# Kernel tuning notes

Hardware: AMD Instinct MI355X
Metric: run time of the kernel (lower is better)

The kernel has to match this reference:

```python
import jax, jax.numpy as jnp
import numpy as np
from jax import lax

B, C, O, K, KS, H, W = 16, 256, 256, 4, 3, 64, 64
PAD = 1
BN_EPS = 1e-3


def setup_inputs() -> dict:
    key = jax.random.key(0)
    k1, k2, k3 = jax.random.split(key, 3)
    x = jax.random.normal(k1, (B, C, H, W), dtype=jnp.float32)
    # nn.Parameter(torch.randn(...)) -> standard normal init
    dyn_kernels = jax.random.normal(k2, (K, O, C, KS, KS), dtype=jnp.float32)
    # attention 1x1 conv (no bias): weight [K, C, 1, 1] -> store as [K, C]
    attn_w = jax.random.normal(k3, (K, C), dtype=jnp.float32) / np.sqrt(C).astype(np.float32)
    gamma = jnp.ones((O,), dtype=jnp.float32)
    beta = jnp.zeros((O,), dtype=jnp.float32)
    return {"x": x, "dyn_kernels": dyn_kernels, "attn_w": attn_w, "gamma": gamma, "beta": beta}


def reference(x, dyn_kernels, attn_w, gamma, beta):
    b, c, h, w = x.shape
    k, o = dyn_kernels.shape[0], dyn_kernels.shape[1]
    # attention: global avg pool -> 1x1 conv (no bias) -> softmax over kernels
    pooled = x.mean(axis=(2, 3))                      # [B, C]
    attn = jax.nn.softmax(pooled @ attn_w.T, axis=1)  # [B, K]
    # run all K kernels as a single conv with K*O output channels
    kern = dyn_kernels.reshape(k * o, c, KS, KS)
    y = lax.conv_general_dilated(
        x, kern, window_strides=(1, 1), padding=((PAD, PAD), (PAD, PAD)),
        dimension_numbers=("NCHW", "OIHW", "NCHW"))   # [B, K*O, H, W]
    y = y.reshape(b, k, o, h, w)
    out = jnp.einsum("bkohw,bk->bohw", y, attn)        # weighted sum over kernels
    # BatchNorm2d (training mode: batch statistics, biased variance)
    mean = out.mean(axis=(0, 2, 3))
    var = out.var(axis=(0, 2, 3))
    inv = gamma * lax.rsqrt(var + BN_EPS)
    out = (out - mean[None, :, None, None]) * inv[None, :, None, None] + beta[None, :, None, None]
    # SiLU
    return out * jax.nn.sigmoid(out)
```

## Files before the change

### kernel.cpp

```cpp
#include <hip/hip_runtime.h>
#include <math.h>


#define B_ 16
#define C_ 256
#define O_ 256
#define HW_ 4096
#define PLANE_F4 1024
#define WPERK 589824
#define XS_PX 40

typedef short bf16x8 __attribute__((ext_vector_type(8)));
typedef float f32x16 __attribute__((ext_vector_type(16)));

__device__ __forceinline__ unsigned short f2bf(float f) {
    unsigned u = __float_as_uint(f);
    u += 0x7FFFu + ((u >> 16) & 1u);
    return (unsigned short)(u >> 16);
}
__device__ __forceinline__ float bf2f(unsigned short h) {
    return __uint_as_float((unsigned)h << 16);
}

__global__ __launch_bounds__(256) void pool_kernel(const float4* __restrict__ x4,
                                                   float* __restrict__ pooled) {
    int bc = blockIdx.x;
    const float4* p = x4 + (size_t)bc * PLANE_F4;
    float s = 0.f;
    for (int i = threadIdx.x; i < PLANE_F4; i += 256) {
        float4 v = p[i];
        s += v.x + v.y + v.z + v.w;
    }
    for (int off = 32; off; off >>= 1) s += __shfl_down(s, off);
    __shared__ float partial[4];
    if ((threadIdx.x & 63) == 0) partial[threadIdx.x >> 6] = s;
    __syncthreads();
    if (threadIdx.x == 0)
        pooled[bc] = (partial[0] + partial[1] + partial[2] + partial[3]) * (1.f / 4096.f);
}

__global__ void attn_kernel(const float* __restrict__ pooled,
                            const float* __restrict__ attn_w,
                            float* __restrict__ attn) {
    int tid = threadIdx.x;
    int b = tid >> 2, k = tid & 3;
    float s = 0.f;
    for (int c = 0; c < C_; ++c) s += pooled[b * C_ + c] * attn_w[k * C_ + c];
    __shared__ float lg[16][4];
    lg[b][k] = s;
    __syncthreads();
    float m = fmaxf(fmaxf(lg[b][0], lg[b][1]), fmaxf(lg[b][2], lg[b][3]));
    float den = expf(lg[b][0] - m) + expf(lg[b][1] - m) +
                expf(lg[b][2] - m) + expf(lg[b][3] - m);
    attn[tid] = expf(s - m) / den;
}

__global__ __launch_bounds__(256) void wtrans_kernel(const float* __restrict__ dyn,
                                                     const float* __restrict__ attn,
                                                     unsigned short* __restrict__ wt_hi,
                                                     unsigned short* __restrict__ wt_lo) {
    int idx = blockIdx.x * 256 + threadIdx.x;
    int b = idx >> 16;
    int o = (idx >> 8) & 255;
    int c = idx & 255;
    float a0 = attn[b * 4 + 0], a1 = attn[b * 4 + 1],
          a2 = attn[b * 4 + 2], a3 = attn[b * 4 + 3];
    const float* p0 = dyn + ((size_t)o * 256 + c) * 9;
    float v[9];
#pragma unroll
    for (int t = 0; t < 9; ++t)
        v[t] = a0 * p0[t] + a1 * p0[WPERK + t] + a2 * p0[2 * WPERK + t] + a3 * p0[3 * WPERK + t];
    size_t obase = ((size_t)(b * 256 + o) * 9) * 256 + c;
#pragma unroll
    for (int t = 0; t < 9; ++t) {
        float f = v[t];
        unsigned short h = f2bf(f);
        unsigned short l = f2bf(f - bf2f(h));
        wt_hi[obase + (size_t)t * 256] = h;
        wt_lo[obase + (size_t)t * 256] = l;
    }
}

__global__ __launch_bounds__(256, 2) void conv_mfma_kernel(const float* __restrict__ x,
        const unsigned short* __restrict__ wt_hi,
        const unsigned short* __restrict__ wt_lo,
        float* __restrict__ out) {
    __shared__ __align__(16) unsigned short xs_hi[4 * 66 * XS_PX];
    __shared__ __align__(16) unsigned short xs_lo[4 * 66 * XS_PX];

    const int bid = blockIdx.x;
    const int swz = (bid & 7) * 128 + (bid >> 3);
    const int b  = swz >> 6;
    const int ob = (swz >> 5) & 1;
    const int hp = swz & 31;
    const int h0 = hp * 2;

    const int tid  = threadIdx.x;
    const int lane = tid & 63;
    const int wid  = tid >> 6;
    const int l31  = lane & 31;
    const int g2   = lane >> 5;
    const int wo   = ob * 128 + (wid >> 1) * 64;
    const int wrow = wid & 1;
    const int hr   = h0 + wrow;

    const int sr = wid;
    const int sw = lane;
    const int hh = h0 - 1 + sr;
    const bool hvalid = (unsigned)hh < 64u;
    const float* xsrc = x + (size_t)b * (C_ * HW_) + (size_t)(hvalid ? hh : 0) * 64 + sw;
    unsigned short* sh_hi = &xs_hi[(sr * 66 + sw + 1) * XS_PX];
    unsigned short* sh_lo = &xs_lo[(sr * 66 + sw + 1) * XS_PX];

    if (tid < 8) {
        int r = tid >> 1;
        int slot = r * 66 + ((tid & 1) ? 65 : 0);
        uint4 z = make_uint4(0u, 0u, 0u, 0u);
#pragma unroll
        for (int u = 0; u < 4; ++u) {
            *(uint4*)&xs_hi[slot * XS_PX + u * 8] = z;
            *(uint4*)&xs_lo[slot * XS_PX + u * 8] = z;
        }
    }

    f32x16 acc[2][2];
#pragma unroll
    for (int i = 0; i < 2; ++i)
#pragma unroll
        for (int j = 0; j < 2; ++j) acc[i][j] = (f32x16)(0.f);

    const unsigned short* wbh = wt_hi + ((size_t)(b * 256 + wo + l31) * 9) * 256 + g2 * 8;
    const unsigned short* wbl = wt_lo + ((size_t)(b * 256 + wo + l31) * 9) * 256 + g2 * 8;
    const unsigned short* xph = xs_hi + (wrow * 66 + l31) * XS_PX + g2 * 8;
    const unsigned short* xpl = xs_lo + (wrow * 66 + l31) * XS_PX + g2 * 8;

#define LOADX(buf, cb) do {                                              \
        const float* _p = xsrc + (size_t)(cb) * HW_;                     \
        if (hvalid) {                                                    \
            _Pragma("unroll")                                            \
            for (int _c = 0; _c < 32; ++_c) buf[_c] = _p[(size_t)_c * HW_]; \
        } else {                                                         \
            _Pragma("unroll")                                            \
            for (int _c = 0; _c < 32; ++_c) buf[_c] = 0.f;               \
        }                                                                \
    } while (0)

#define STOREX(buf) do {                                                 \
        unsigned _hw[16], _lw[16];                                       \
        _Pragma("unroll")                                                \
        for (int _c = 0; _c < 16; ++_c) {                                \
            unsigned short h0_ = f2bf(buf[2 * _c]);                      \
            unsigned short l0_ = f2bf(buf[2 * _c] - bf2f(h0_));          \
            unsigned short h1_ = f2bf(buf[2 * _c + 1]);                  \
            unsigned short l1_ = f2bf(buf[2 * _c + 1] - bf2f(h1_));      \
            _hw[_c] = (unsigned)h0_ | ((unsigned)h1_ << 16);             \
            _lw[_c] = (unsigned)l0_ | ((unsigned)l1_ << 16);             \
        }                                                                \
        _Pragma("unroll")                                                \
        for (int _u = 0; _u < 4; ++_u) {                                 \
            *(uint4*)&sh_hi[_u * 8] = make_uint4(_hw[4*_u], _hw[4*_u+1], _hw[4*_u+2], _hw[4*_u+3]); \
            *(uint4*)&sh_lo[_u * 8] = make_uint4(_lw[4*_u], _lw[4*_u+1], _lw[4*_u+2], _lw[4*_u+3]); \
        }                                                                \
    } while (0)

#define MFMA_CHUNK(cb) do {                                              \
        _Pragma("unroll")                                                \
        for (int t = 0; t < 9; ++t) {                                    \
            const int dh = t / 3, dw = t % 3;                            \
            bf16x8 bh_[2][2], bl_[2][2];                                 \
            _Pragma("unroll")                                            \
            for (int ks = 0; ks < 2; ++ks)                               \
                _Pragma("unroll")                                        \
                for (int nf = 0; nf < 2; ++nf) {                         \
                    const int xoff = (dh * 66 + dw + nf * 32) * XS_PX + ks * 16; \
                    bh_[ks][nf] = *(const bf16x8*)&xph[xoff];            \
                    bl_[ks][nf] = *(const bf16x8*)&xpl[xoff];            \
                }                                                        \
            bf16x8 ah_[2][2], al_[2][2];                                 \
            _Pragma("unroll")                                            \
            for (int mf = 0; mf < 2; ++mf)                               \
                _Pragma("unroll")                                        \
                for (int ks = 0; ks < 2; ++ks) {                         \
                    const size_t woff = (size_t)mf * 73728 + (size_t)t * 256 + ks * 16 + (cb); \
                    ah_[mf][ks] = *(const bf16x8*)(wbh + woff);          \
                    al_[mf][ks] = *(const bf16x8*)(wbl + woff);          \
                }                                                        \
            _Pragma("unroll")                                            \
            for (int mf = 0; mf < 2; ++mf)                               \
                _Pragma("unroll")                                        \
                for (int ks = 0; ks < 2; ++ks)                           \
                    _Pragma("unroll")                                    \
                    for (int nf = 0; nf < 2; ++nf)                       \
                        acc[mf][nf] = __builtin_amdgcn_mfma_f32_32x32x16_bf16(ah_[mf][ks], bh_[ks][nf], acc[mf][nf], 0, 0, 0); \
            _Pragma("unroll")                                            \
            for (int mf = 0; mf < 2; ++mf)                               \
                _Pragma("unroll")                                        \
                for (int ks = 0; ks < 2; ++ks)                           \
                    _Pragma("unroll")                                    \
                    for (int nf = 0; nf < 2; ++nf)                       \
                        acc[mf][nf] = __builtin_amdgcn_mfma_f32_32x32x16_bf16(ah_[mf][ks], bl_[ks][nf], acc[mf][nf], 0, 0, 0); \
            _Pragma("unroll")                                            \
            for (int mf = 0; mf < 2; ++mf)                               \
                _Pragma("unroll")                                        \
                for (int ks = 0; ks < 2; ++ks)                           \
                    _Pragma("unroll")                                    \
                    for (int nf = 0; nf < 2; ++nf)                       \
                        acc[mf][nf] = __builtin_amdgcn_mfma_f32_32x32x16_bf16(al_[mf][ks], bh_[ks][nf], acc[mf][nf], 0, 0, 0); \
        }                                                                \
    } while (0)

    float xa[32], xb2[32];
    LOADX(xa, 0);
#pragma unroll 1
    for (int cc = 0; cc < 256; cc += 64) {
        __syncthreads();
        STOREX(xa);
        __syncthreads();
        LOADX(xb2, cc + 32);
        MFMA_CHUNK(cc);
        __syncthreads();
        STOREX(xb2);
        __syncthreads();
        if (cc + 64 < 256) LOADX(xa, cc + 64);
        MFMA_CHUNK(cc + 32);
    }

    float* op = out + ((size_t)b * 256 + wo) * HW_ + (size_t)hr * 64;
#pragma unroll
    for (int mf = 0; mf < 2; ++mf)
#pragma unroll
        for (int nf = 0; nf < 2; ++nf) {
            f32x16 a = acc[mf][nf];
#pragma unroll
            for (int r = 0; r < 16; ++r) {
                int row = (r & 3) + 8 * (r >> 2) + 4 * g2;
                op[(size_t)(mf * 32 + row) * HW_ + nf * 32 + l31] = a[r];
            }
        }
#undef LOADX
#undef STOREX
#undef MFMA_CHUNK
}

__global__ __launch_bounds__(256, 2) void conv_otf_kernel(const float* __restrict__ x,
                                                          const float* __restrict__ wsrc,
                                                          const float* __restrict__ attn,
                                                          float* __restrict__ out) {
    __shared__ __align__(16) float xs[8][3][72];
    __shared__ __align__(16) float wsh[64 * 100];
    const int h   = blockIdx.x;
    const int ob  = blockIdx.y * 64;
    const int b   = blockIdx.z;
    const int tid = threadIdx.x;
    const int o_idx = tid >> 4;
    const int w0    = (tid & 15) * 4;
    float a0 = attn[b * 4 + 0], a1 = attn[b * 4 + 1],
          a2 = attn[b * 4 + 2], a3 = attn[b * 4 + 3];
    const float* xb = x + (size_t)b * (C_ * HW_);
    const float* wb = wsrc + (size_t)ob * 2304;
    float acc[4][4];
#pragma unroll
    for (int i = 0; i < 4; ++i)
#pragma unroll
        for (int j = 0; j < 4; ++j) acc[i][j] = 0.f;
    for (int cb = 0; cb < C_; cb += 8) {
        __syncthreads();
        for (int idx = tid; idx < 8 * 3 * 66; idx += 256) {
            int c = idx / 198, rem = idx - c * 198;
            int r = rem / 66, wi = rem - r * 66;
            int hhh = h - 1 + r, ww = wi - 1;
            float v = 0.f;
            if ((unsigned)hhh < 64u && (unsigned)ww < 64u)
                v = xb[(size_t)(cb + c) * HW_ + hhh * 64 + ww];
            xs[c][r][wi] = v;
        }
        for (int idx = tid; idx < 64 * 72; idx += 256) {
            int o = idx / 72, j = idx - o * 72;
            int c = j / 9, t = j - c * 9;
            size_t gi = (size_t)o * 2304 + (size_t)(cb + c) * 9 + t;
            float v = a0 * wb[gi] + a1 * wb[WPERK + gi] +
                      a2 * wb[2 * WPERK + gi] + a3 * wb[3 * WPERK + gi];
            wsh[o * 100 + c * 12 + t] = v;
        }
        __syncthreads();
#pragma unroll
        for (int cc = 0; cc < 8; ++cc) {
            float xr[3][6];
#pragma unroll
            for (int r = 0; r < 3; ++r) {
                float4 a = *(const float4*)&xs[cc][r][w0];
                float2 b2 = *(const float2*)&xs[cc][r][w0 + 4];
                xr[r][0] = a.x; xr[r][1] = a.y; xr[r][2] = a.z; xr[r][3] = a.w;
                xr[r][4] = b2.x; xr[r][5] = b2.y;
            }
#pragma unroll
            for (int oo = 0; oo < 4; ++oo) {
                const float* wp = &wsh[(o_idx * 4 + oo) * 100 + cc * 12];
                float4 wA = *(const float4*)wp;
                float4 wB = *(const float4*)(wp + 4);
                float w8 = wp[8];
#pragma unroll
                for (int ww = 0; ww < 4; ++ww) {
                    acc[oo][ww] += wA.x * xr[0][ww]     + wA.y * xr[0][ww + 1] + wA.z * xr[0][ww + 2]
                                 + wA.w * xr[1][ww]     + wB.x * xr[1][ww + 1] + wB.y * xr[1][ww + 2]
                                 + wB.z * xr[2][ww]     + wB.w * xr[2][ww + 1] + w8   * xr[2][ww + 2];
                }
            }
        }
    }
    float* op = out + ((size_t)b * O_ + ob) * HW_ + h * 64;
#pragma unroll
    for (int oo = 0; oo < 4; ++oo) {
        float4 v = make_float4(acc[oo][0], acc[oo][1], acc[oo][2], acc[oo][3]);
        *(float4*)&op[(size_t)(o_idx * 4 + oo) * HW_ + w0] = v;
    }
}

__global__ __launch_bounds__(256) void stats1_kernel(const float4* __restrict__ out4,
                                                     float* __restrict__ psum,
                                                     float* __restrict__ psumsq) {
    int bo = blockIdx.x;
    const float4* p = out4 + (size_t)bo * PLANE_F4;
    float s = 0.f, s2 = 0.f;
    for (int i = threadIdx.x; i < PLANE_F4; i += 256) {
        float4 v = p[i];
        s  += v.x + v.y + v.z + v.w;
        s2 += v.x * v.x + v.y * v.y + v.z * v.z + v.w * v.w;
    }
    for (int off = 32; off; off >>= 1) {
        s  += __shfl_down(s, off);
        s2 += __shfl_down(s2, off);
    }
    __shared__ float ps[4], ps2[4];
    int w = threadIdx.x >> 6;
    if ((threadIdx.x & 63) == 0) { ps[w] = s; ps2[w] = s2; }
    __syncthreads();
    if (threadIdx.x == 0) {
        psum[bo]   = ps[0] + ps[1] + ps[2] + ps[3];
        psumsq[bo] = ps2[0] + ps2[1] + ps2[2] + ps2[3];
    }
}

__global__ __launch_bounds__(256) void stats2_kernel(const float* __restrict__ psum,
                                                     const float* __restrict__ psumsq,
                                                     const float* __restrict__ gamma,
                                                     float* __restrict__ mean,
                                                     float* __restrict__ inv) {
    int o = threadIdx.x;
    float S = 0.f, S2 = 0.f;
#pragma unroll
    for (int b = 0; b < B_; ++b) {
        S  += psum[b * 256 + o];
        S2 += psumsq[b * 256 + o];
    }
    float m = S * (1.f / 65536.f);
    float var = S2 * (1.f / 65536.f) - m * m;
    mean[o] = m;
    inv[o] = gamma[o] * rsqrtf(var + 1e-3f);
}

__global__ __launch_bounds__(256) void bn_silu_kernel(float4* __restrict__ out4,
                                                      const float* __restrict__ mean,
                                                      const float* __restrict__ inv,
                                                      const float* __restrict__ beta) {
    const int total = B_ * O_ * PLANE_F4;
    for (int i = blockIdx.x * 256 + threadIdx.x; i < total; i += gridDim.x * 256) {
        int plane = i >> 10;
        int o = plane & 255;
        float m = mean[o], iv = inv[o], bt = beta[o];
        float4 v = out4[i];
        float u;
        u = (v.x - m) * iv + bt; v.x = u / (1.f + expf(-u));
        u = (v.y - m) * iv + bt; v.y = u / (1.f + expf(-u));
        u = (v.z - m) * iv + bt; v.z = u / (1.f + expf(-u));
        u = (v.w - m) * iv + bt; v.w = u / (1.f + expf(-u));
        out4[i] = v;
    }
}

extern "C" void kernel_launch(void* const* d_in, const int* in_sizes, int n_in,
                              void* d_out, int out_size, void* d_ws, size_t ws_size,
                              hipStream_t stream) {
    const float* x      = (const float*)d_in[0];
    const float* dyn    = (const float*)d_in[1];
    const float* attn_w = (const float*)d_in[2];
    const float* gamma  = (const float*)d_in[3];
    const float* beta   = (const float*)d_in[4];
    float* out = (float*)d_out;
    float* ws  = (float*)d_ws;

    float* pooled = ws;
    float* attn   = ws + 4096;
    float* mean   = ws + 4160;
    float* inv    = ws + 4416;
    unsigned short* wt_hi = (unsigned short*)(ws + 4672);
    unsigned short* wt_lo = wt_hi + 9437184;
    float* psum   = (float*)wt_hi;
    float* psumsq = psum + 4096;

    const size_t needed = (size_t)4672 * 4 + 2ull * 9437184ull * 2ull;
    const bool mfma_path = ws_size >= needed;

    pool_kernel<<<4096, 256, 0, stream>>>((const float4*)x, pooled);
    attn_kernel<<<1, 64, 0, stream>>>(pooled, attn_w, attn);
    if (mfma_path) {
        wtrans_kernel<<<4096, 256, 0, stream>>>(dyn, attn, wt_hi, wt_lo);
        conv_mfma_kernel<<<1024, 256, 0, stream>>>(x, wt_hi, wt_lo, out);
    } else {
        conv_otf_kernel<<<dim3(64, 4, 16), 256, 0, stream>>>(x, dyn, attn, out);
    }
    stats1_kernel<<<4096, 256, 0, stream>>>((const float4*)out, psum, psumsq);
    stats2_kernel<<<1, 256, 0, stream>>>(psum, psumsq, gamma, mean, inv);
    bn_silu_kernel<<<4096, 256, 0, stream>>>((float4*)out, mean, inv, beta);
}
```

Baseline: 450.0 us.

## Fuse BN statistics into MFMA conv epilogue and retile conv to one row per block

The conv kernel now handles one output row with all 256 output channels per block (four waves of 64 channels each) and stages a 3-row halo, so each block loads the x tile once for every channel. The conv epilogue computes per-channel partial sums and sums of squares from the accumulators and writes them to a workspace, and a small reduce kernel turns them into mean and inverse std. This removes the full re-read of the conv output by the old stats kernel. It also adds s_setprio around the MFMA groups and reorders the MFMA loops. The fused path needs extra workspace; when that space is missing it falls back to a single-kernel stats pass.

```diff
diff --git a/kernel.cpp b/kernel.cpp
--- a/kernel.cpp
+++ b/kernel.cpp
@@ -81,47 +81,37 @@
     }
 }
 
+template <bool FUSED_STATS>
 __global__ __launch_bounds__(256, 2) void conv_mfma_kernel(const float* __restrict__ x,
         const unsigned short* __restrict__ wt_hi,
         const unsigned short* __restrict__ wt_lo,
-        float* __restrict__ out) {
-    __shared__ __align__(16) unsigned short xs_hi[4 * 66 * XS_PX];
-    __shared__ __align__(16) unsigned short xs_lo[4 * 66 * XS_PX];
+        float* __restrict__ out,
+        float* __restrict__ psum,
+        float* __restrict__ psumsq) {
+    __shared__ __align__(16) unsigned short xs_hi[3 * 66 * XS_PX];
+    __shared__ __align__(16) unsigned short xs_lo[3 * 66 * XS_PX];
 
     const int bid = blockIdx.x;
-    const int swz = (bid & 7) * 128 + (bid >> 3);
-    const int b  = swz >> 6;
-    const int ob = (swz >> 5) & 1;
-    const int hp = swz & 31;
-    const int h0 = hp * 2;
+    const int wk  = (bid & 7) * 128 + (bid >> 3);
+    const int b   = wk >> 6;
+    const int h   = wk & 63;
 
     const int tid  = threadIdx.x;
     const int lane = tid & 63;
     const int wid  = tid >> 6;
     const int l31  = lane & 31;
     const int g2   = lane >> 5;
-    const int wo   = ob * 128 + (wid >> 1) * 64;
-    const int wrow = wid & 1;
-    const int hr   = h0 + wrow;
-
-    const int sr = wid;
-    const int sw = lane;
-    const int hh = h0 - 1 + sr;
-    const bool hvalid = (unsigned)hh < 64u;
-    const float* xsrc = x + (size_t)b * (C_ * HW_) + (size_t)(hvalid ? hh : 0) * 64 + sw;
-    unsigned short* sh_hi = &xs_hi[(sr * 66 + sw + 1) * XS_PX];
-    unsigned short* sh_lo = &xs_lo[(sr * 66 + sw + 1) * XS_PX];
-
-    if (tid < 8) {
-        int r = tid >> 1;
-        int slot = r * 66 + ((tid & 1) ? 65 : 0);
-        uint4 z = make_uint4(0u, 0u, 0u, 0u);
-#pragma unroll
-        for (int u = 0; u < 4; ++u) {
-            *(uint4*)&xs_hi[slot * XS_PX + u * 8] = z;
-            *(uint4*)&xs_lo[slot * XS_PX + u * 8] = z;
-        }
-    }
+    const int wo   = wid * 64;
+
+    const int sr = tid / 66;
+    const int sw = tid - sr * 66;
+    const bool sactive = tid < 198;
+    const int hh = h - 1 + sr;
+    const int ww = sw - 1;
+    const bool svalid = sactive && (unsigned)hh < 64u && (unsigned)ww < 64u;
+    const float* xsrc = x + (size_t)b * (C_ * HW_) + (size_t)(svalid ? hh : 0) * 64 + (svalid ? ww : 0);
+    unsigned short* sh_hi = &xs_hi[(sr * 66 + sw) * XS_PX];
+    unsigned short* sh_lo = &xs_lo[(sr * 66 + sw) * XS_PX];
 
     f32x16 acc[2][2];
 #pragma unroll
@@ -131,12 +121,12 @@
 
     const unsigned short* wbh = wt_hi + ((size_t)(b * 256 + wo + l31) * 9) * 256 + g2 * 8;
     const unsigned short* wbl = wt_lo + ((size_t)(b * 256 + wo + l31) * 9) * 256 + g2 * 8;
-    const unsigned short* xph = xs_hi + (wrow * 66 + l31) * XS_PX + g2 * 8;
-    const unsigned short* xpl = xs_lo + (wrow * 66 + l31) * XS_PX + g2 * 8;
+    const unsigned short* xph = xs_hi + l31 * XS_PX + g2 * 8;
+    const unsigned short* xpl = xs_lo + l31 * XS_PX + g2 * 8;
 
 #define LOADX(buf, cb) do {                                              \
-        const float* _p = xsrc + (size_t)(cb) * HW_;                     \
-        if (hvalid) {                                                    \
+        if (svalid) {                                                    \
+            const float* _p = xsrc + (size_t)(cb) * HW_;                 \
             _Pragma("unroll")                                            \
             for (int _c = 0; _c < 32; ++_c) buf[_c] = _p[(size_t)_c * HW_]; \
         } else {                                                         \
@@ -146,20 +136,22 @@
     } while (0)
 
 #define STOREX(buf) do {                                                 \
-        unsigned _hw[16], _lw[16];                                       \
-        _Pragma("unroll")                                                \
-        for (int _c = 0; _c < 16; ++_c) {                                \
-            unsigned short h0_ = f2bf(buf[2 * _c]);                      \
-            unsigned short l0_ = f2bf(buf[2 * _c] - bf2f(h0_));          \
-            unsigned short h1_ = f2bf(buf[2 * _c + 1]);                  \
-            unsigned short l1_ = f2bf(buf[2 * _c + 1] - bf2f(h1_));      \
-            _hw[_c] = (unsigned)h0_ | ((unsigned)h1_ << 16);             \
-            _lw[_c] = (unsigned)l0_ | ((unsigned)l1_ << 16);             \
-        }                                                                \
-        _Pragma("unroll")                                                \
-        for (int _u = 0; _u < 4; ++_u) {                                 \
-            *(uint4*)&sh_hi[_u * 8] = make_uint4(_hw[4*_u], _hw[4*_u+1], _hw[4*_u+2], _hw[4*_u+3]); \
-            *(uint4*)&sh_lo[_u * 8] = make_uint4(_lw[4*_u], _lw[4*_u+1], _lw[4*_u+2], _lw[4*_u+3]); \
+        if (sactive) {                                                   \
+            unsigned _hw[16], _lw[16];                                   \
+            _Pragma("unroll")                                            \
+            for (int _c = 0; _c < 16; ++_c) {                            \
+                unsigned short h0_ = f2bf(buf[2 * _c]);                  \
+                unsigned short l0_ = f2bf(buf[2 * _c] - bf2f(h0_));      \
+                unsigned short h1_ = f2bf(buf[2 * _c + 1]);              \
+                unsigned short l1_ = f2bf(buf[2 * _c + 1] - bf2f(h1_));  \
+                _hw[_c] = (unsigned)h0_ | ((unsigned)h1_ << 16);         \
+                _lw[_c] = (unsigned)l0_ | ((unsigned)l1_ << 16);         \
+            }                                                            \
+            _Pragma("unroll")                                            \
+            for (int _u = 0; _u < 4; ++_u) {                             \
+                *(uint4*)&sh_hi[_u * 8] = make_uint4(_hw[4*_u], _hw[4*_u+1], _hw[4*_u+2], _hw[4*_u+3]); \
+                *(uint4*)&sh_lo[_u * 8] = make_uint4(_lw[4*_u], _lw[4*_u+1], _lw[4*_u+2], _lw[4*_u+3]); \
+            }                                                            \
         }                                                                \
     } while (0)
 
@@ -185,27 +177,29 @@
                     ah_[mf][ks] = *(const bf16x8*)(wbh + woff);          \
                     al_[mf][ks] = *(const bf16x8*)(wbl + woff);          \
                 }                                                        \
-            _Pragma("unroll")                                            \
-            for (int mf = 0; mf < 2; ++mf)                               \
+            __builtin_amdgcn_s_setprio(1);                               \
+            _Pragma("unroll")                                            \
+            for (int ks = 0; ks < 2; ++ks)                               \
                 _Pragma("unroll")                                        \
-                for (int ks = 0; ks < 2; ++ks)                           \
+                for (int mf = 0; mf < 2; ++mf)                           \
                     _Pragma("unroll")                                    \
                     for (int nf = 0; nf < 2; ++nf)                       \
                         acc[mf][nf] = __builtin_amdgcn_mfma_f32_32x32x16_bf16(ah_[mf][ks], bh_[ks][nf], acc[mf][nf], 0, 0, 0); \
             _Pragma("unroll")                                            \
-            for (int mf = 0; mf < 2; ++mf)                               \
+            for (int ks = 0; ks < 2; ++ks)                               \
                 _Pragma("unroll")                                        \
-                for (int ks = 0; ks < 2; ++ks)                           \
+                for (int mf = 0; mf < 2; ++mf)                           \
                     _Pragma("unroll")                                    \
                     for (int nf = 0; nf < 2; ++nf)                       \
                         acc[mf][nf] = __builtin_amdgcn_mfma_f32_32x32x16_bf16(ah_[mf][ks], bl_[ks][nf], acc[mf][nf], 0, 0, 0); \
             _Pragma("unroll")                                            \
-            for (int mf = 0; mf < 2; ++mf)                               \
+            for (int ks = 0; ks < 2; ++ks)                               \
                 _Pragma("unroll")                                        \
-                for (int ks = 0; ks < 2; ++ks)                           \
+                for (int mf = 0; mf < 2; ++mf)                           \
                     _Pragma("unroll")                                    \
                     for (int nf = 0; nf < 2; ++nf)                       \
                         acc[mf][nf] = __builtin_amdgcn_mfma_f32_32x32x16_bf16(al_[mf][ks], bh_[ks][nf], acc[mf][nf], 0, 0, 0); \
+            __builtin_amdgcn_s_setprio(0);                               \
         }                                                                \
     } while (0)
 
@@ -225,7 +219,7 @@
         MFMA_CHUNK(cc + 32);
     }
 
-    float* op = out + ((size_t)b * 256 + wo) * HW_ + (size_t)hr * 64;
+    float* op = out + ((size_t)b * 256 + wo) * HW_ + (size_t)h * 64;
 #pragma unroll
     for (int mf = 0; mf < 2; ++mf)
 #pragma unroll
@@ -237,6 +231,27 @@
                 op[(size_t)(mf * 32 + row) * HW_ + nf * 32 + l31] = a[r];
             }
         }
+
+    if (FUSED_STATS) {
+#pragma unroll
+        for (int mf = 0; mf < 2; ++mf)
+#pragma unroll
+            for (int r = 0; r < 16; ++r) {
+                float v0 = acc[mf][0][r], v1 = acc[mf][1][r];
+                float s = v0 + v1;
+                float q = v0 * v0 + v1 * v1;
+#pragma unroll
+                for (int off = 1; off < 32; off <<= 1) {
+                    s += __shfl_xor(s, off);
+                    q += __shfl_xor(q, off);
+                }
+                if (l31 == 0) {
+                    int o = wo + mf * 32 + (r & 3) + 8 * (r >> 2) + 4 * g2;
+                    psum[(size_t)o * 1024 + wk] = s;
+                    psumsq[(size_t)o * 1024 + wk] = q;
+                }
+            }
+    }
 #undef LOADX
 #undef STOREX
 #undef MFMA_CHUNK
@@ -316,16 +331,19 @@
     }
 }
 
-__global__ __launch_bounds__(256) void stats1_kernel(const float4* __restrict__ out4,
-                                                     float* __restrict__ psum,
-                                                     float* __restrict__ psumsq) {
-    int bo = blockIdx.x;
-    const float4* p = out4 + (size_t)bo * PLANE_F4;
+__global__ __launch_bounds__(256) void stats_full_kernel(const float4* __restrict__ out4,
+                                                         const float* __restrict__ gamma,
+                                                         float* __restrict__ mean,
+                                                         float* __restrict__ inv) {
+    int o = blockIdx.x;
     float s = 0.f, s2 = 0.f;
-    for (int i = threadIdx.x; i < PLANE_F4; i += 256) {
-        float4 v = p[i];
-        s  += v.x + v.y + v.z + v.w;
-        s2 += v.x * v.x + v.y * v.y + v.z * v.z + v.w * v.w;
+    for (int b = 0; b < B_; ++b) {
+        const float4* p = out4 + ((size_t)b * O_ + o) * PLANE_F4;
+        for (int i = threadIdx.x; i < PLANE_F4; i += 256) {
+            float4 v = p[i];
+            s  += v.x + v.y + v.z + v.w;
+            s2 += v.x * v.x + v.y * v.y + v.z * v.z + v.w * v.w;
+        }
     }
     for (int off = 32; off; off >>= 1) {
         s  += __shfl_down(s, off);
@@ -336,27 +354,41 @@
     if ((threadIdx.x & 63) == 0) { ps[w] = s; ps2[w] = s2; }
     __syncthreads();
     if (threadIdx.x == 0) {
-        psum[bo]   = ps[0] + ps[1] + ps[2] + ps[3];
-        psumsq[bo] = ps2[0] + ps2[1] + ps2[2] + ps2[3];
-    }
-}
-
-__global__ __launch_bounds__(256) void stats2_kernel(const float* __restrict__ psum,
-                                                     const float* __restrict__ psumsq,
-                                                     const float* __restrict__ gamma,
-                                                     float* __restrict__ mean,
-                                                     float* __restrict__ inv) {
-    int o = threadIdx.x;
-    float S = 0.f, S2 = 0.f;
-#pragma unroll
-    for (int b = 0; b < B_; ++b) {
-        S  += psum[b * 256 + o];
-        S2 += psumsq[b * 256 + o];
-    }
-    float m = S * (1.f / 65536.f);
-    float var = S2 * (1.f / 65536.f) - m * m;
-    mean[o] = m;
-    inv[o] = gamma[o] * rsqrtf(var + 1e-3f);
+        float S = ps[0] + ps[1] + ps[2] + ps[3];
+        float S2 = ps2[0] + ps2[1] + ps2[2] + ps2[3];
+        float m = S * (1.f / 65536.f);
+        float var = S2 * (1.f / 65536.f) - m * m;
+        mean[o] = m;
+        inv[o] = gamma[o] * rsqrtf(var + 1e-3f);
+    }
+}
+
+__global__ __launch_bounds__(256) void stats_reduce_kernel(const float* __restrict__ psum,
+                                                           const float* __restrict__ psumsq,
+                                                           const float* __restrict__ gamma,
+                                                           float* __restrict__ mean,
+                                                           float* __restrict__ inv) {
+    int o = blockIdx.x;
+    const float* ps = psum + (size_t)o * 1024;
+    const float* pq = psumsq + (size_t)o * 1024;
+    float s = 0.f, q = 0.f;
+    for (int i = threadIdx.x; i < 1024; i += 256) { s += ps[i]; q += pq[i]; }
+    for (int off = 32; off; off >>= 1) {
+        s += __shfl_down(s, off);
+        q += __shfl_down(q, off);
+    }
+    __shared__ float a[4], b2[4];
+    int w = threadIdx.x >> 6;
+    if ((threadIdx.x & 63) == 0) { a[w] = s; b2[w] = q; }
+    __syncthreads();
+    if (threadIdx.x == 0) {
+        float S = a[0] + a[1] + a[2] + a[3];
+        float Q = b2[0] + b2[1] + b2[2] + b2[3];
+        float m = S * (1.f / 65536.f);
+        float var = Q * (1.f / 65536.f) - m * m;
+        mean[o] = m;
+        inv[o] = gamma[o] * rsqrtf(var + 1e-3f);
+    }
 }
 
 __global__ __launch_bounds__(256) void bn_silu_kernel(float4* __restrict__ out4,
@@ -395,21 +427,28 @@
     float* inv    = ws + 4416;
     unsigned short* wt_hi = (unsigned short*)(ws + 4672);
     unsigned short* wt_lo = wt_hi + 9437184;
-    float* psum   = (float*)wt_hi;
-    float* psumsq = psum + 4096;
-
-    const size_t needed = (size_t)4672 * 4 + 2ull * 9437184ull * 2ull;
-    const bool mfma_path = ws_size >= needed;
+    float* psum   = (float*)(wt_lo + 9437184);
+    float* psumsq = psum + 262144;
+
+    const size_t need_mfma  = (size_t)4672 * 4 + 2ull * 9437184ull * 2ull;
+    const size_t need_fused = need_mfma + 2ull * 262144ull * 4ull;
+    const bool mfma_path = ws_size >= need_mfma;
+    const bool fused     = ws_size >= need_fused;
 
     pool_kernel<<<4096, 256, 0, stream>>>((const float4*)x, pooled);
     attn_kernel<<<1, 64, 0, stream>>>(pooled, attn_w, attn);
     if (mfma_path) {
         wtrans_kernel<<<4096, 256, 0, stream>>>(dyn, attn, wt_hi, wt_lo);
-        conv_mfma_kernel<<<1024, 256, 0, stream>>>(x, wt_hi, wt_lo, out);
+        if (fused) {
+            conv_mfma_kernel<true><<<1024, 256, 0, stream>>>(x, wt_hi, wt_lo, out, psum, psumsq);
+            stats_reduce_kernel<<<256, 256, 0, stream>>>(psum, psumsq, gamma, mean, inv);
+        } else {
+            conv_mfma_kernel<false><<<1024, 256, 0, stream>>>(x, wt_hi, wt_lo, out, psum, psumsq);
+            stats_full_kernel<<<256, 256, 0, stream>>>((const float4*)out, gamma, mean, inv);
+        }
     } else {
         conv_otf_kernel<<<dim3(64, 4, 16), 256, 0, stream>>>(x, dyn, attn, out);
-    }
-    stats1_kernel<<<4096, 256, 0, stream>>>((const float4*)out, psum, psumsq);
-    stats2_kernel<<<1, 256, 0, stream>>>(psum, psumsq, gamma, mean, inv);
+        stats_full_kernel<<<256, 256, 0, stream>>>((const float4*)out, gamma, mean, inv);
+    }
     bn_silu_kernel<<<4096, 256, 0, stream>>>((float4*)out, mean, inv, beta);
 }
```

New measurement: 462.0 us. +2.7%, slower.
